# Kernel optimization log

Hardware: AMD Instinct MI355X
Metric: run time of the kernel (lower is better)

The kernel has to match this reference:

```python
import jax, jax.numpy as jnp
import numpy as np

S, T, D, H = 16384, 16, 128, 3   # statements, AST nodes per statement, feat dim, heads
N = S * T
EPS = 1e-5


def setup_inputs() -> dict:
    key = jax.random.key(0)
    k = jax.random.split(key, 12)
    idx = np.arange(N)
    child = idx[idx % T != 0]                      # chain edges child->parent within each AST
    src = jnp.asarray(np.concatenate([child, idx]), dtype=jnp.int32)       # + self loops
    dst = jnp.asarray(np.concatenate([child - 1, idx]), dtype=jnp.int32)
    sD = 1.0 / np.sqrt(D)
    s3D = 1.0 / np.sqrt(3.0 * D)
    return dict(
        x=jax.random.normal(k[0], (N, D), jnp.float32),
        W0=jax.random.normal(k[1], (D, H * D), jnp.float32) * sD,
        a_src0=jax.random.normal(k[2], (H, D), jnp.float32) * sD,
        a_dst0=jax.random.normal(k[3], (H, D), jnp.float32) * sD,
        b0=jnp.zeros((H * D,), jnp.float32),
        g0=jnp.ones((H * D,), jnp.float32),
        be0=jnp.zeros((H * D,), jnp.float32),
        W1=jax.random.normal(k[4], (H * D, D), jnp.float32) * s3D,
        a_src1=jax.random.normal(k[5], (1, D), jnp.float32) * sD,
        a_dst1=jax.random.normal(k[6], (1, D), jnp.float32) * sD,
        b1=jnp.zeros((D,), jnp.float32),
        g1=jnp.ones((D,), jnp.float32),
        be1=jnp.zeros((D,), jnp.float32),
        p=jax.random.normal(k[7], (D,), jnp.float32),
        mW1=jax.random.normal(k[8], (D, 32), jnp.float32) * sD,
        mb1=jnp.zeros((32,), jnp.float32),
        mW2=jax.random.normal(k[9], (32, D), jnp.float32) / np.sqrt(32.0),
        mb2=jnp.zeros((D,), jnp.float32),
        src=src,
        dst=dst,
    )


def _gat(x, W, a_s, a_d, b, src, dst, heads, out_c):
    # PyG GATConv (concat heads, leaky_relu 0.2, self-loops already in edge list)
    h = (x @ W).reshape(-1, heads, out_c)                 # [N,H,C]
    al_s = jnp.einsum('nhc,hc->nh', h, a_s)
    al_d = jnp.einsum('nhc,hc->nh', h, a_d)
    e = jax.nn.leaky_relu(al_s[src] + al_d[dst], 0.2)     # [E,H]
    m = jax.ops.segment_max(e, dst, num_segments=N)       # segment softmax over incoming edges
    ex = jnp.exp(e - m[dst])
    den = jax.ops.segment_sum(ex, dst, num_segments=N)
    alpha = ex / den[dst]
    out = jax.ops.segment_sum(alpha[:, :, None] * h[src], dst, num_segments=N)
    return out.reshape(-1, heads * out_c) + b


def _bn(x, g, b):
    mu = x.mean(0)
    var = x.var(0)
    return (x - mu) * jax.lax.rsqrt(var + EPS) * g + b


def reference(x, W0, a_src0, a_dst0, b0, g0, be0, W1, a_src1, a_dst1, b1, g1, be1, p, mW1, mb1, mW2, mb2, src, dst):
    h = _bn(jax.nn.relu(_gat(x, W0, a_src0, a_dst0, b0, src, dst, H, D)), g0, be0)
    h = _bn(jax.nn.relu(_gat(h, W1, a_src1, a_dst1, b1, src, dst, 1, D)), g1, be1)
    # TopKPooling (default ratio=0.5) per statement AST of T nodes
    s = (h @ p) / (jnp.linalg.norm(p) + 1e-16)            # [N]
    s = s.reshape(S, T)
    k = T // 2
    vals, idxk = jax.lax.top_k(s, k)                      # [S,k]
    hr = h.reshape(S, T, D)
    sel = jnp.take_along_axis(hr, idxk[:, :, None], axis=1) * jnp.tanh(vals)[:, :, None]
    pooled = jax.nn.relu(sel).mean(axis=1)                # [S,D] readout of kept nodes
    out = jax.nn.relu(pooled @ mW1 + mb1) @ mW2 + mb2     # MLP 128->32->128
    return out
```

## Files before the change

### kernel.cpp

```cpp
#include <hip/hip_runtime.h>
#include <math.h>

#define N_NODES 262144
#define SSTMT   16384
#define TT      16
#define DD      128
#define HH      3
#define HD      384
#define EPSV    1e-5f

__device__ __forceinline__ int swzc(int row, int c) { return c ^ (((row >> 3) & 3) << 2); }

template<int NTHR>
__device__ __forceinline__ void stageSwz(float (*dst)[DD], const float* __restrict__ src)
{
    const int tid = threadIdx.x;
    #pragma unroll
    for (int j = 0; j < 2048 / NTHR; ++j) {
        int gi = j * NTHR + tid;
        int row = gi >> 5;
        int c4 = (gi & 31) * 4;
        *reinterpret_cast<float4*>(&dst[row][swzc(row, c4)]) =
            *reinterpret_cast<const float4*>(&src[(size_t)row * DD + c4]);
    }
}

template<int BSTR, int KLEN>
__device__ __forceinline__ void gemm8x8(const float (*A)[DD], const float* __restrict__ Bbase,
                                        int kbeg, int rr, int pad, float acc[8][8])
{
    const float* bp = Bbase + (size_t)kbeg * BSTR;
    const float* ar = &A[rr * 8][0];
    #pragma unroll 2
    for (int k = 0; k < KLEN; k += 4) {
        float4 b00 = *reinterpret_cast<const float4*>(bp);
        float4 b01 = *reinterpret_cast<const float4*>(bp + 4);
        float4 b10 = *reinterpret_cast<const float4*>(bp + BSTR);
        float4 b11 = *reinterpret_cast<const float4*>(bp + BSTR + 4);
        float4 b20 = *reinterpret_cast<const float4*>(bp + 2 * BSTR);
        float4 b21 = *reinterpret_cast<const float4*>(bp + 2 * BSTR + 4);
        float4 b30 = *reinterpret_cast<const float4*>(bp + 3 * BSTR);
        float4 b31 = *reinterpret_cast<const float4*>(bp + 3 * BSTR + 4);
        bp += 4 * (size_t)BSTR;
        const int pc = (kbeg + k) ^ pad;
        #pragma unroll
        for (int i = 0; i < 8; ++i) {
            float4 a = *reinterpret_cast<const float4*>(ar + i * DD + pc);
            acc[i][0] += a.x*b00.x; acc[i][1] += a.x*b00.y; acc[i][2] += a.x*b00.z; acc[i][3] += a.x*b00.w;
            acc[i][4] += a.x*b01.x; acc[i][5] += a.x*b01.y; acc[i][6] += a.x*b01.z; acc[i][7] += a.x*b01.w;
            acc[i][0] += a.y*b10.x; acc[i][1] += a.y*b10.y; acc[i][2] += a.y*b10.z; acc[i][3] += a.y*b10.w;
            acc[i][4] += a.y*b11.x; acc[i][5] += a.y*b11.y; acc[i][6] += a.y*b11.z; acc[i][7] += a.y*b11.w;
            acc[i][0] += a.z*b20.x; acc[i][1] += a.z*b20.y; acc[i][2] += a.z*b20.z; acc[i][3] += a.z*b20.w;
            acc[i][4] += a.z*b21.x; acc[i][5] += a.z*b21.y; acc[i][6] += a.z*b21.z; acc[i][7] += a.z*b21.w;
            acc[i][0] += a.w*b30.x; acc[i][1] += a.w*b30.y; acc[i][2] += a.w*b30.z; acc[i][3] += a.w*b30.w;
            acc[i][4] += a.w*b31.x; acc[i][5] += a.w*b31.y; acc[i][6] += a.w*b31.z; acc[i][7] += a.w*b31.w;
        }
    }
}

__device__ __forceinline__ void attnAgg(float acc[8][8],
                                        const float* __restrict__ avsP,
                                        const float* __restrict__ avdP,
                                        const float* __restrict__ bP, int rr)
{
    float4 s0 = *reinterpret_cast<const float4*>(avsP);
    float4 s1 = *reinterpret_cast<const float4*>(avsP + 4);
    float4 d0 = *reinterpret_cast<const float4*>(avdP);
    float4 d1 = *reinterpret_cast<const float4*>(avdP + 4);
    float als[8], ald[8];
    #pragma unroll
    for (int i = 0; i < 8; ++i) {
        als[i] = acc[i][0]*s0.x + acc[i][1]*s0.y + acc[i][2]*s0.z + acc[i][3]*s0.w
               + acc[i][4]*s1.x + acc[i][5]*s1.y + acc[i][6]*s1.z + acc[i][7]*s1.w;
        ald[i] = acc[i][0]*d0.x + acc[i][1]*d0.y + acc[i][2]*d0.z + acc[i][3]*d0.w
               + acc[i][4]*d1.x + acc[i][5]*d1.y + acc[i][6]*d1.z + acc[i][7]*d1.w;
    }
    #pragma unroll
    for (int m = 1; m <= 8; m <<= 1) {
        #pragma unroll
        for (int i = 0; i < 8; ++i) {
            als[i] += __shfl_xor(als[i], m);
            ald[i] += __shfl_xor(ald[i], m);
        }
    }
    float alsN = __shfl_down(als[0], 16);
    float accN[8];
    #pragma unroll
    for (int j = 0; j < 8; ++j) accN[j] = __shfl_down(acc[0][j], 16);

    float4 bb0 = *reinterpret_cast<const float4*>(bP);
    float4 bb1 = *reinterpret_cast<const float4*>(bP + 4);
    float bbv[8] = {bb0.x, bb0.y, bb0.z, bb0.w, bb1.x, bb1.y, bb1.z, bb1.w};
    const bool tail7 = (rr & 1);
    #pragma unroll
    for (int i = 0; i < 8; ++i) {
        float es = als[i] + ald[i];
        es = es > 0.f ? es : 0.2f * es;
        float aS = 1.f, aN = 0.f;
        if (!(tail7 && i == 7)) {
            float en = ((i < 7) ? als[i + 1] : alsN) + ald[i];
            en = en > 0.f ? en : 0.2f * en;
            float mx = fmaxf(es, en);
            float e1 = expf(es - mx), e2 = expf(en - mx);
            float den = e1 + e2;
            aS = e1 / den; aN = e2 / den;
        }
        #pragma unroll
        for (int j = 0; j < 8; ++j) {
            float nb = (i < 7) ? acc[i + 1][j] : accN[j];
            acc[i][j] = fmaxf(aS * acc[i][j] + aN * nb + bbv[j], 0.f);
        }
    }
}

__global__ __launch_bounds__(128, 2)
void gat0_stats(const float* __restrict__ x, const float* __restrict__ W0,
                const float* __restrict__ as0, const float* __restrict__ ad0,
                const float* __restrict__ b0, float* __restrict__ pA0)
{
    __shared__ float xs[64][DD];
    __shared__ float bns[8][DD];

    const int tid = threadIdx.x;
    const int bid = blockIdx.x;
    const int rr = tid >> 4;
    const int cg = tid & 15;
    const int pad = (rr & 3) << 2;
    const size_t rb = (size_t)bid * 64;

    stageSwz<128>(xs, x + rb * DD);
    __syncthreads();

    for (int h = 0; h < HH; ++h) {
        float acc[8][8];
        #pragma unroll
        for (int i = 0; i < 8; ++i)
            #pragma unroll
            for (int j = 0; j < 8; ++j) acc[i][j] = 0.f;

        gemm8x8<HD, 128>(xs, W0 + h * DD + cg * 8, 0, rr, pad, acc);
        attnAgg(acc, as0 + h * DD + cg * 8, ad0 + h * DD + cg * 8, b0 + h * DD + cg * 8, rr);

        float ps[8], pq[8];
        #pragma unroll
        for (int j = 0; j < 8; ++j) { ps[j] = 0.f; pq[j] = 0.f; }
        #pragma unroll
        for (int i = 0; i < 8; ++i)
            #pragma unroll
            for (int j = 0; j < 8; ++j) {
                float o = acc[i][j];
                ps[j] += o; pq[j] += o * o;
            }

        __syncthreads();
        *reinterpret_cast<float4*>(&bns[rr][cg * 8]) =
            make_float4(ps[0], ps[1], ps[2], ps[3]);
        *reinterpret_cast<float4*>(&bns[rr][cg * 8 + 4]) =
            make_float4(ps[4], ps[5], ps[6], ps[7]);
        __syncthreads();
        float sv = 0.f;
        #pragma unroll
        for (int w = 0; w < 8; ++w) sv += bns[w][tid];
        __syncthreads();
        *reinterpret_cast<float4*>(&bns[rr][cg * 8]) =
            make_float4(pq[0], pq[1], pq[2], pq[3]);
        *reinterpret_cast<float4*>(&bns[rr][cg * 8 + 4]) =
            make_float4(pq[4], pq[5], pq[6], pq[7]);
        __syncthreads();
        float qv = 0.f;
        #pragma unroll
        for (int w = 0; w < 8; ++w) qv += bns[w][tid];
        size_t idx = ((size_t)bid * HD + h * DD + tid) * 2;
        pA0[idx] = sv; pA0[idx + 1] = qv;
    }
}

__global__ __launch_bounds__(256, 2)
void gat1_recomp(const float* __restrict__ x, const float* __restrict__ W0,
                 const float* __restrict__ as0, const float* __restrict__ ad0,
                 const float* __restrict__ b0, const float* __restrict__ sc0,
                 const float* __restrict__ sh0, const float* __restrict__ W1,
                 const float* __restrict__ as1, const float* __restrict__ ad1,
                 const float* __restrict__ b1,
                 float* __restrict__ r1, float* __restrict__ pA1)
{
    __shared__ float xs[64][DD];
    __shared__ float hs[64][DD];
    __shared__ float bps[8][DD], bqs[8][DD];

    const int tid = threadIdx.x;
    const int bid = blockIdx.x;
    const int kh = tid >> 7;
    const int rr = (tid >> 4) & 7;
    const int cg = tid & 15;
    const int pad = (rr & 3) << 2;
    const size_t rb = (size_t)bid * 64;
    const bool finisher = (kh == ((rr >= 4) ? 1 : 0));

    stageSwz<256>(xs, x + rb * DD);
    __syncthreads();

    float acc2[8][8];
    #pragma unroll
    for (int i = 0; i < 8; ++i)
        #pragma unroll
        for (int j = 0; j < 8; ++j) acc2[i][j] = 0.f;

    for (int h = 0; h < HH; ++h) {
        float acc[8][8];
        #pragma unroll
        for (int i = 0; i < 8; ++i)
            #pragma unroll
            for (int j = 0; j < 8; ++j) acc[i][j] = 0.f;

        gemm8x8<HD, 64>(xs, W0 + h * DD + cg * 8, kh * 64, rr, pad, acc);

        __syncthreads();
        if (!finisher) {
            #pragma unroll
            for (int i = 0; i < 8; ++i) {
                int pc = (cg * 8) ^ pad;
                *reinterpret_cast<float4*>(&hs[rr * 8 + i][pc]) =
                    make_float4(acc[i][0], acc[i][1], acc[i][2], acc[i][3]);
                *reinterpret_cast<float4*>(&hs[rr * 8 + i][pc ^ 4]) =
                    make_float4(acc[i][4], acc[i][5], acc[i][6], acc[i][7]);
            }
        }
        __syncthreads();
        if (finisher) {
            #pragma unroll
            for (int i = 0; i < 8; ++i) {
                int pc = (cg * 8) ^ pad;
                float4 p0 = *reinterpret_cast<const float4*>(&hs[rr * 8 + i][pc]);
                float4 p1 = *reinterpret_cast<const float4*>(&hs[rr * 8 + i][pc ^ 4]);
                acc[i][0] += p0.x; acc[i][1] += p0.y; acc[i][2] += p0.z; acc[i][3] += p0.w;
                acc[i][4] += p1.x; acc[i][5] += p1.y; acc[i][6] += p1.z; acc[i][7] += p1.w;
            }
            attnAgg(acc, as0 + h * DD + cg * 8, ad0 + h * DD + cg * 8, b0 + h * DD + cg * 8, rr);
            float4 sc0a = *reinterpret_cast<const float4*>(&sc0[h * DD + cg * 8]);
            float4 sc0b = *reinterpret_cast<const float4*>(&sc0[h * DD + cg * 8 + 4]);
            float4 sh0a = *reinterpret_cast<const float4*>(&sh0[h * DD + cg * 8]);
            float4 sh0b = *reinterpret_cast<const float4*>(&sh0[h * DD + cg * 8 + 4]);
            float scv[8] = {sc0a.x, sc0a.y, sc0a.z, sc0a.w, sc0b.x, sc0b.y, sc0b.z, sc0b.w};
            float shv[8] = {sh0a.x, sh0a.y, sh0a.z, sh0a.w, sh0b.x, sh0b.y, sh0b.z, sh0b.w};
            #pragma unroll
            for (int i = 0; i < 8; ++i) {
                int pc = (cg * 8) ^ pad;
                float v0 = acc[i][0] * scv[0] + shv[0];
                float v1 = acc[i][1] * scv[1] + shv[1];
                float v2 = acc[i][2] * scv[2] + shv[2];
                float v3 = acc[i][3] * scv[3] + shv[3];
                float v4 = acc[i][4] * scv[4] + shv[4];
                float v5 = acc[i][5] * scv[5] + shv[5];
                float v6 = acc[i][6] * scv[6] + shv[6];
                float v7 = acc[i][7] * scv[7] + shv[7];
                *reinterpret_cast<float4*>(&hs[rr * 8 + i][pc]) = make_float4(v0, v1, v2, v3);
                *reinterpret_cast<float4*>(&hs[rr * 8 + i][pc ^ 4]) = make_float4(v4, v5, v6, v7);
            }
        }
        __syncthreads();

        gemm8x8<DD, 64>(hs, W1 + (size_t)(h * DD) * DD + cg * 8, kh * 64, rr, pad, acc2);
    }

    __syncthreads();
    if (!finisher) {
        #pragma unroll
        for (int i = 0; i < 8; ++i) {
            int pc = (cg * 8) ^ pad;
            *reinterpret_cast<float4*>(&xs[rr * 8 + i][pc]) =
                make_float4(acc2[i][0], acc2[i][1], acc2[i][2], acc2[i][3]);
            *reinterpret_cast<float4*>(&xs[rr * 8 + i][pc ^ 4]) =
                make_float4(acc2[i][4], acc2[i][5], acc2[i][6], acc2[i][7]);
        }
    }
    __syncthreads();
    if (finisher) {
        #pragma unroll
        for (int i = 0; i < 8; ++i) {
            int pc = (cg * 8) ^ pad;
            float4 p0 = *reinterpret_cast<const float4*>(&xs[rr * 8 + i][pc]);
            float4 p1 = *reinterpret_cast<const float4*>(&xs[rr * 8 + i][pc ^ 4]);
            acc2[i][0] += p0.x; acc2[i][1] += p0.y; acc2[i][2] += p0.z; acc2[i][3] += p0.w;
            acc2[i][4] += p1.x; acc2[i][5] += p1.y; acc2[i][6] += p1.z; acc2[i][7] += p1.w;
        }
        attnAgg(acc2, as1 + cg * 8, ad1 + cg * 8, b1 + cg * 8, rr);

        float ps[8], pq[8];
        #pragma unroll
        for (int j = 0; j < 8; ++j) { ps[j] = 0.f; pq[j] = 0.f; }
        #pragma unroll
        for (int i = 0; i < 8; ++i) {
            *reinterpret_cast<float4*>(&r1[(rb + rr * 8 + i) * DD + cg * 8]) =
                make_float4(acc2[i][0], acc2[i][1], acc2[i][2], acc2[i][3]);
            *reinterpret_cast<float4*>(&r1[(rb + rr * 8 + i) * DD + cg * 8 + 4]) =
                make_float4(acc2[i][4], acc2[i][5], acc2[i][6], acc2[i][7]);
            #pragma unroll
            for (int j = 0; j < 8; ++j) { ps[j] += acc2[i][j]; pq[j] += acc2[i][j] * acc2[i][j]; }
        }
        *reinterpret_cast<float4*>(&bps[rr][cg * 8])     = make_float4(ps[0], ps[1], ps[2], ps[3]);
        *reinterpret_cast<float4*>(&bps[rr][cg * 8 + 4]) = make_float4(ps[4], ps[5], ps[6], ps[7]);
        *reinterpret_cast<float4*>(&bqs[rr][cg * 8])     = make_float4(pq[0], pq[1], pq[2], pq[3]);
        *reinterpret_cast<float4*>(&bqs[rr][cg * 8 + 4]) = make_float4(pq[4], pq[5], pq[6], pq[7]);
    }
    __syncthreads();
    if (tid < 128) {
        float s = 0.f, q = 0.f;
        #pragma unroll
        for (int w = 0; w < 8; ++w) { s += bps[w][tid]; q += bqs[w][tid]; }
        size_t idx = ((size_t)bid * DD + tid) * 2;
        pA1[idx] = s; pA1[idx + 1] = q;
    }
}

__global__ __launch_bounds__(256)
void bn_reduce(const float* __restrict__ pA, int nblk, int ncol, float invN,
               const float* __restrict__ g, const float* __restrict__ be,
               float* __restrict__ sc, float* __restrict__ sh)
{
    __shared__ float rs[256], rq[256];
    int col = blockIdx.x, tid = threadIdx.x;
    float s = 0.f, q = 0.f;
    for (int i = tid; i < nblk; i += 256) {
        size_t idx = ((size_t)i * ncol + col) * 2;
        s += pA[idx]; q += pA[idx + 1];
    }
    rs[tid] = s; rq[tid] = q;
    __syncthreads();
    for (int o = 128; o > 0; o >>= 1) {
        if (tid < o) { rs[tid] += rs[tid + o]; rq[tid] += rq[tid + o]; }
        __syncthreads();
    }
    if (tid == 0) {
        float mu  = rs[0] * invN;
        float var = fmaxf(rq[0] * invN - mu * mu, 0.f);
        float inv = 1.0f / sqrtf(var + EPSV);
        float scv = g[col] * inv;
        sc[col] = scv;
        sh[col] = be[col] - mu * scv;
    }
}

__global__ __launch_bounds__(128)
void compute_pn(const float* __restrict__ p, float* __restrict__ pn)
{
    __shared__ float rs[128];
    int t = threadIdx.x;
    float v = p[t];
    rs[t] = v * v;
    __syncthreads();
    for (int o = 64; o > 0; o >>= 1) {
        if (t < o) rs[t] += rs[t + o];
        __syncthreads();
    }
    float nrm = sqrtf(rs[0]) + 1e-16f;
    pn[t] = v / nrm;
}

__global__ __launch_bounds__(128)
void pool_mlp(const float* __restrict__ r1, const float* __restrict__ sc1,
              const float* __restrict__ sh1, const float* __restrict__ pn,
              const float* __restrict__ mW1, const float* __restrict__ mb1,
              const float* __restrict__ mW2, const float* __restrict__ mb2,
              float* __restrict__ out)
{
    __shared__ float hf[16][136];
    __shared__ float sv[16];
    __shared__ float tv[16];
    __shared__ float pooled[128];
    __shared__ float y1[32];
    int tid = threadIdx.x;
    int sid = blockIdx.x;
    float scv = sc1[tid], shv = sh1[tid];
    const float* base = r1 + (size_t)sid * TT * DD;
    #pragma unroll
    for (int i = 0; i < 16; ++i)
        hf[i][tid] = base[i * DD + tid] * scv + shv;
    __syncthreads();

    {
        int r = tid >> 3, q = tid & 7;
        float s = 0.f;
        #pragma unroll
        for (int cc = 0; cc < 16; ++cc) {
            int c = q + cc * 8;
            s += hf[r][c] * pn[c];
        }
        s += __shfl_down(s, 4, 8);
        s += __shfl_down(s, 2, 8);
        s += __shfl_down(s, 1, 8);
        if (q == 0) sv[r] = s;
    }
    __syncthreads();

    if (tid < 16) {
        float si = sv[tid];
        int rank = 0;
        #pragma unroll
        for (int u = 0; u < 16; ++u) {
            float su = sv[u];
            rank += (su > si || (su == si && u < tid)) ? 1 : 0;
        }
        tv[tid] = (rank < 8) ? tanhf(si) : 0.f;
    }
    __syncthreads();

    {
        float a = 0.f;
        #pragma unroll
        for (int rr2 = 0; rr2 < 16; ++rr2)
            a += fmaxf(hf[rr2][tid] * tv[rr2], 0.f);
        pooled[tid] = a * 0.125f;
    }
    __syncthreads();

    {
        int j = tid >> 2, q = tid & 3;
        float a = 0.f;
        #pragma unroll
        for (int cc = 0; cc < 32; ++cc) {
            int c = q + cc * 4;
            a += pooled[c] * mW1[(size_t)c * 32 + j];
        }
        a += __shfl_down(a, 2, 4);
        a += __shfl_down(a, 1, 4);
        if (q == 0) y1[j] = fmaxf(a + mb1[j], 0.f);
    }
    __syncthreads();

    {
        float o = mb2[tid];
        #pragma unroll
        for (int j = 0; j < 32; ++j) o += y1[j] * mW2[j * 128 + tid];
        out[(size_t)sid * 128 + tid] = o;
    }
}

extern "C" void kernel_launch(void* const* d_in, const int* in_sizes, int n_in,
                              void* d_out, int out_size, void* d_ws, size_t ws_size,
                              hipStream_t stream)
{
    (void)in_sizes; (void)n_in; (void)out_size; (void)ws_size;
    const float* x   = (const float*)d_in[0];
    const float* W0  = (const float*)d_in[1];
    const float* as0 = (const float*)d_in[2];
    const float* ad0 = (const float*)d_in[3];
    const float* b0  = (const float*)d_in[4];
    const float* g0  = (const float*)d_in[5];
    const float* be0 = (const float*)d_in[6];
    const float* W1  = (const float*)d_in[7];
    const float* as1 = (const float*)d_in[8];
    const float* ad1 = (const float*)d_in[9];
    const float* b1  = (const float*)d_in[10];
    const float* g1  = (const float*)d_in[11];
    const float* be1 = (const float*)d_in[12];
    const float* p   = (const float*)d_in[13];
    const float* mW1 = (const float*)d_in[14];
    const float* mb1 = (const float*)d_in[15];
    const float* mW2 = (const float*)d_in[16];
    const float* mb2 = (const float*)d_in[17];
    float* out = (float*)d_out;

    const size_t R1B  = (size_t)N_NODES * DD * 4;
    const size_t PA0B = 4096ull * HD * 2 * 4;
    const size_t PA1B = 4096ull * DD * 2 * 4;

    char* ws = (char*)d_ws;
    float* r1  = (float*)ws;
    float* pA0 = (float*)(ws + R1B);
    float* pA1 = (float*)(ws + R1B + PA0B);
    float* vec = (float*)(ws + R1B + PA0B + PA1B);
    float* sc0 = vec;
    float* sh0 = vec + 512;
    float* sc1 = vec + 1024;
    float* sh1 = vec + 1536;
    float* pn  = vec + 2048;

    const float invN = 1.0f / (float)N_NODES;

    gat0_stats<<<N_NODES / 64, 128, 0, stream>>>(x, W0, as0, ad0, b0, pA0);
    bn_reduce<<<HD, 256, 0, stream>>>(pA0, N_NODES / 64, HD, invN, g0, be0, sc0, sh0);
    compute_pn<<<1, 128, 0, stream>>>(p, pn);
    gat1_recomp<<<N_NODES / 64, 256, 0, stream>>>(x, W0, as0, ad0, b0, sc0, sh0,
                                                  W1, as1, ad1, b1, r1, pA1);
    bn_reduce<<<DD, 256, 0, stream>>>(pA1, N_NODES / 64, DD, invN, g1, be1, sc1, sh1);
    pool_mlp<<<SSTMT, 128, 0, stream>>>(r1, sc1, sh1, pn, mW1, mb1, mW2, mb2, out);
}
```

Measured before the change: 1.068 ms.

## Use split-bf16 MFMA for layer-0 GEMM in the BN statistics pass

Replaces the FP32 SIMT GEMM in the first GAT-layer statistics kernel with bf16 MFMA instructions. Both operands are split into three bf16 parts (hi/mid/lo), and six cross-product MFMAs per tile emulate FP32 accuracy. A new prep kernel transposes W0 and splits it into bf16 planes. The attention coefficients and BN partial sums are now computed through a shared-memory staging buffer with more synchronisation. This adds per-call conversion work and six MFMA passes, and the gat1_recomp kernel still uses the old FP32 path.

After: 1.290 ms. +20.8%, slower.

```diff
diff --git a/kernel.cpp b/kernel.cpp
--- a/kernel.cpp
+++ b/kernel.cpp
@@ -8,6 +8,196 @@
 #define HH      3
 #define HD      384
 #define EPSV    1e-5f
+
+typedef __attribute__((ext_vector_type(8))) short short8v;
+typedef __attribute__((ext_vector_type(4))) float f32x4;
+
+__device__ __forceinline__ short bf16rne(float x){
+    unsigned u = __float_as_uint(x);
+    unsigned r = (u + 0x7FFFu + ((u >> 16) & 1u)) >> 16;
+    return (short)r;
+}
+__device__ __forceinline__ float bf2f(short s){
+    return __uint_as_float(((unsigned)(unsigned short)s) << 16);
+}
+
+__global__ __launch_bounds__(128)
+void prep_w0t(const float* __restrict__ W0, short* __restrict__ w0t)
+{
+    int c = blockIdx.x;
+    int k = threadIdx.x;
+    float v = W0[(size_t)k * HD + c];
+    short hi = bf16rne(v);
+    float r1 = v - bf2f(hi);
+    short mi = bf16rne(r1);
+    float r2 = r1 - bf2f(mi);
+    short lo = bf16rne(r2);
+    size_t idx = (size_t)c * 128 + k;
+    w0t[idx]          = hi;
+    w0t[49152 + idx]  = mi;
+    w0t[98304 + idx]  = lo;
+}
+
+__global__ __launch_bounds__(256, 2)
+void gat0_stats_mfma(const float* __restrict__ x, const short* __restrict__ w0t,
+                     const float* __restrict__ as0, const float* __restrict__ ad0,
+                     const float* __restrict__ b0, float* __restrict__ pA0)
+{
+    __shared__ short xpl[3][64][128];
+    __shared__ float hbuf[32][128];
+    __shared__ float avs[128], avd[128];
+    __shared__ float als[32], ald[32], aSw[32], aNw[32];
+
+    const int tid = threadIdx.x;
+    const int bid = blockIdx.x;
+    const size_t rb = (size_t)bid * 64;
+    const int l = tid & 63;
+    const int w = tid >> 6;
+
+    for (int ch = 0; ch < 4; ++ch) {
+        int gi = ch * 256 + tid;
+        int row = gi >> 4;
+        int c8 = (gi & 15) * 8;
+        const float* xp = x + (rb + row) * DD + c8;
+        short8v hi, mi, lo;
+        #pragma unroll
+        for (int j = 0; j < 8; ++j) {
+            float v = xp[j];
+            short h_ = bf16rne(v);
+            float r1 = v - bf2f(h_);
+            short m_ = bf16rne(r1);
+            float r2 = r1 - bf2f(m_);
+            hi[j] = h_; mi[j] = m_; lo[j] = bf16rne(r2);
+        }
+        int dc = c8 ^ ((row & 7) << 3);
+        *reinterpret_cast<short8v*>(&xpl[0][row][dc]) = hi;
+        *reinterpret_cast<short8v*>(&xpl[1][row][dc]) = mi;
+        *reinterpret_cast<short8v*>(&xpl[2][row][dc]) = lo;
+    }
+    __syncthreads();
+
+    const int mt  = w & 1;
+    const int nt0 = (w >> 1) * 4;
+    const int arow_l = mt * 16 + (l & 15);
+    const int akb = (l >> 4) * 8;
+    const int bl16 = l & 15;
+    const int bk   = (l >> 4) * 8;
+
+    for (int h = 0; h < HH; ++h) {
+        if (tid < 128) { avs[tid] = as0[h * DD + tid]; avd[tid] = ad0[h * DD + tid]; }
+        float ps[4] = {0, 0, 0, 0}, pq[4] = {0, 0, 0, 0};
+
+        for (int half = 0; half < 2; ++half) {
+            const int arow = half * 32 + arow_l;
+
+            f32x4 acc[4];
+            #pragma unroll
+            for (int t = 0; t < 4; ++t) acc[t] = (f32x4){0.f, 0.f, 0.f, 0.f};
+
+            #pragma unroll
+            for (int kc = 0; kc < 4; ++kc) {
+                int ke = kc * 32 + akb;
+                int sc_ = ke ^ ((arow & 7) << 3);
+                short8v ahi = *reinterpret_cast<const short8v*>(&xpl[0][arow][sc_]);
+                short8v ami = *reinterpret_cast<const short8v*>(&xpl[1][arow][sc_]);
+                short8v alo = *reinterpret_cast<const short8v*>(&xpl[2][arow][sc_]);
+                #pragma unroll
+                for (int t = 0; t < 4; ++t) {
+                    int bcol = h * DD + (nt0 + t) * 16 + bl16;
+                    const short* bb = w0t + (size_t)bcol * 128 + kc * 32 + bk;
+                    short8v bhi = *reinterpret_cast<const short8v*>(bb);
+                    short8v bmi = *reinterpret_cast<const short8v*>(bb + 49152);
+                    short8v blo = *reinterpret_cast<const short8v*>(bb + 98304);
+                    acc[t] = __builtin_amdgcn_mfma_f32_16x16x32_bf16(ahi, bhi, acc[t], 0, 0, 0);
+                    acc[t] = __builtin_amdgcn_mfma_f32_16x16x32_bf16(ahi, bmi, acc[t], 0, 0, 0);
+                    acc[t] = __builtin_amdgcn_mfma_f32_16x16x32_bf16(ami, bhi, acc[t], 0, 0, 0);
+                    acc[t] = __builtin_amdgcn_mfma_f32_16x16x32_bf16(ahi, blo, acc[t], 0, 0, 0);
+                    acc[t] = __builtin_amdgcn_mfma_f32_16x16x32_bf16(ami, bmi, acc[t], 0, 0, 0);
+                    acc[t] = __builtin_amdgcn_mfma_f32_16x16x32_bf16(alo, bhi, acc[t], 0, 0, 0);
+                }
+            }
+
+            __syncthreads();
+            #pragma unroll
+            for (int t = 0; t < 4; ++t) {
+                int col = (nt0 + t) * 16 + (l & 15);
+                int rw = mt * 16 + (l >> 4) * 4;
+                hbuf[rw + 0][col] = acc[t][0];
+                hbuf[rw + 1][col] = acc[t][1];
+                hbuf[rw + 2][col] = acc[t][2];
+                hbuf[rw + 3][col] = acc[t][3];
+            }
+            __syncthreads();
+
+            if (tid < 64) {
+                int r = tid & 31;
+                const float* av = (tid < 32) ? avs : avd;
+                float s = 0.f;
+                #pragma unroll 8
+                for (int cc = 0; cc < 128; ++cc) {
+                    int c = (cc + r * 4) & 127;
+                    s += hbuf[r][c] * av[c];
+                }
+                if (tid < 32) als[r] = s; else ald[r] = s;
+            }
+            __syncthreads();
+            if (tid < 32) {
+                int r = tid;
+                float es = als[r] + ald[r];
+                es = es > 0.f ? es : 0.2f * es;
+                float aSv = 1.f, aNv = 0.f;
+                if ((r & 15) != 15) {
+                    float en = als[r + 1] + ald[r];
+                    en = en > 0.f ? en : 0.2f * en;
+                    float mx = fmaxf(es, en);
+                    float e1 = expf(es - mx), e2 = expf(en - mx);
+                    float dn = e1 + e2;
+                    aSv = e1 / dn; aNv = e2 / dn;
+                }
+                aSw[r] = aSv; aNw[r] = aNv;
+            }
+            __syncthreads();
+
+            {
+                int rg = tid >> 5, c4g = (tid & 31) * 4;
+                float4 bb4 = *reinterpret_cast<const float4*>(&b0[h * DD + c4g]);
+                float bbv[4] = {bb4.x, bb4.y, bb4.z, bb4.w};
+                #pragma unroll
+                for (int i = 0; i < 4; ++i) {
+                    int r = rg * 4 + i;
+                    float a_s = aSw[r], a_n = aNw[r];
+                    bool hasn = ((r & 15) != 15);
+                    #pragma unroll
+                    for (int j = 0; j < 4; ++j) {
+                        float v = hbuf[r][c4g + j];
+                        if (hasn) v = a_s * v + a_n * hbuf[r + 1][c4g + j];
+                        float o = fmaxf(v + bbv[j], 0.f);
+                        ps[j] += o; pq[j] += o * o;
+                    }
+                }
+            }
+        }
+
+        float* bna = &hbuf[0][0];
+        __syncthreads();
+        {
+            int rg = tid >> 5, c4g = (tid & 31) * 4;
+            #pragma unroll
+            for (int j = 0; j < 4; ++j) {
+                bna[rg * 128 + c4g + j] = ps[j];
+                bna[1024 + rg * 128 + c4g + j] = pq[j];
+            }
+        }
+        __syncthreads();
+        if (tid < 128) {
+            float s = 0.f, q = 0.f;
+            #pragma unroll
+            for (int g = 0; g < 8; ++g) { s += bna[g * 128 + tid]; q += bna[1024 + g * 128 + tid]; }
+            size_t idx = ((size_t)bid * HD + h * DD + tid) * 2;
+            pA0[idx] = s; pA0[idx + 1] = q;
+        }
+    }
+}
 
 __device__ __forceinline__ int swzc(int row, int c) { return c ^ (((row >> 3) & 3) << 2); }
 
@@ -110,68 +300,6 @@
             float nb = (i < 7) ? acc[i + 1][j] : accN[j];
             acc[i][j] = fmaxf(aS * acc[i][j] + aN * nb + bbv[j], 0.f);
         }
-    }
-}
-
-__global__ __launch_bounds__(128, 2)
-void gat0_stats(const float* __restrict__ x, const float* __restrict__ W0,
-                const float* __restrict__ as0, const float* __restrict__ ad0,
-                const float* __restrict__ b0, float* __restrict__ pA0)
-{
-    __shared__ float xs[64][DD];
-    __shared__ float bns[8][DD];
-
-    const int tid = threadIdx.x;
-    const int bid = blockIdx.x;
-    const int rr = tid >> 4;
-    const int cg = tid & 15;
-    const int pad = (rr & 3) << 2;
-    const size_t rb = (size_t)bid * 64;
-
-    stageSwz<128>(xs, x + rb * DD);
-    __syncthreads();
-
-    for (int h = 0; h < HH; ++h) {
-        float acc[8][8];
-        #pragma unroll
-        for (int i = 0; i < 8; ++i)
-            #pragma unroll
-            for (int j = 0; j < 8; ++j) acc[i][j] = 0.f;
-
-        gemm8x8<HD, 128>(xs, W0 + h * DD + cg * 8, 0, rr, pad, acc);
-        attnAgg(acc, as0 + h * DD + cg * 8, ad0 + h * DD + cg * 8, b0 + h * DD + cg * 8, rr);
-
-        float ps[8], pq[8];
-        #pragma unroll
-        for (int j = 0; j < 8; ++j) { ps[j] = 0.f; pq[j] = 0.f; }
-        #pragma unroll
-        for (int i = 0; i < 8; ++i)
-            #pragma unroll
-            for (int j = 0; j < 8; ++j) {
-                float o = acc[i][j];
-                ps[j] += o; pq[j] += o * o;
-            }
-
-        __syncthreads();
-        *reinterpret_cast<float4*>(&bns[rr][cg * 8]) =
-            make_float4(ps[0], ps[1], ps[2], ps[3]);
-        *reinterpret_cast<float4*>(&bns[rr][cg * 8 + 4]) =
-            make_float4(ps[4], ps[5], ps[6], ps[7]);
-        __syncthreads();
-        float sv = 0.f;
-        #pragma unroll
-        for (int w = 0; w < 8; ++w) sv += bns[w][tid];
-        __syncthreads();
-        *reinterpret_cast<float4*>(&bns[rr][cg * 8]) =
-            make_float4(pq[0], pq[1], pq[2], pq[3]);
-        *reinterpret_cast<float4*>(&bns[rr][cg * 8 + 4]) =
-            make_float4(pq[4], pq[5], pq[6], pq[7]);
-        __syncthreads();
-        float qv = 0.f;
-        #pragma unroll
-        for (int w = 0; w < 8; ++w) qv += bns[w][tid];
-        size_t idx = ((size_t)bid * HD + h * DD + tid) * 2;
-        pA0[idx] = sv; pA0[idx + 1] = qv;
     }
 }
 
@@ -464,6 +592,7 @@
     const size_t R1B  = (size_t)N_NODES * DD * 4;
     const size_t PA0B = 4096ull * HD * 2 * 4;
     const size_t PA1B = 4096ull * DD * 2 * 4;
+    const size_t VECB = 3072 * 4;
 
     char* ws = (char*)d_ws;
     float* r1  = (float*)ws;
@@ -475,10 +604,12 @@
     float* sc1 = vec + 1024;
     float* sh1 = vec + 1536;
     float* pn  = vec + 2048;
+    short* w0t = (short*)(ws + R1B + PA0B + PA1B + VECB);
 
     const float invN = 1.0f / (float)N_NODES;
 
-    gat0_stats<<<N_NODES / 64, 128, 0, stream>>>(x, W0, as0, ad0, b0, pA0);
+    prep_w0t<<<HD, 128, 0, stream>>>(W0, w0t);
+    gat0_stats_mfma<<<N_NODES / 64, 256, 0, stream>>>(x, w0t, as0, ad0, b0, pA0);
     bn_reduce<<<HD, 256, 0, stream>>>(pA0, N_NODES / 64, HD, invN, g0, be0, sc0, sh0);
     compute_pn<<<1, 128, 0, stream>>>(p, pn);
     gat1_recomp<<<N_NODES / 64, 256, 0, stream>>>(x, W0, as0, ad0, b0, sc0, sh0,
```
